# Kernel tuning notes

Measured on AMD Instinct MI355X. Metric: run time of the kernel, lower is better.

The kernel has to match this reference:

```python
import jax, jax.numpy as jnp
import numpy as np

N, F, H, C = 4096, 128, 32, 205   # nodes, in-features, hidden=32, clusters=ceil(4096/20)
L, T, R = 512, 12, 4              # teams, team size, replaced members per team
EPS_POOL = 1e-15                  # torch_geometric EPS in dense_diff_pool
BN_EPS = 1e-5


def setup_inputs():
    ks = jax.random.split(jax.random.key(0), 12)
    rng = np.random.default_rng(0)
    # distinct node ids per team; replace = first R members, remain = rest
    teams = np.argsort(rng.random((L, N)), axis=1)[:, :T].astype(np.int64)
    g = lambda i, shape, s: jax.random.normal(ks[i], shape, jnp.float32) * s
    D = 2 * H + C  # 269
    return {
        'x': g(0, (N, F), 1.0),
        'adj': jax.random.uniform(ks[1], (1, N, N), jnp.float32),
        'sample_teams': jnp.asarray(teams),
        'sample_replaces': jnp.asarray(teams[:, :R]),
        'W1r': g(2, (F, H), 0.08), 'b1': jnp.zeros((H,), jnp.float32), 'W1root': g(3, (F, H), 0.08),
        'g1': jnp.ones((H,), jnp.float32), 'be1': jnp.zeros((H,), jnp.float32),
        'W2r': g(4, (H, H), 0.17), 'b2': jnp.zeros((H,), jnp.float32), 'W2root': g(5, (H, H), 0.17),
        'g2': jnp.ones((H,), jnp.float32), 'be2': jnp.zeros((H,), jnp.float32),
        'W3r': g(6, (H, C), 0.17), 'b3': jnp.zeros((C,), jnp.float32), 'W3root': g(7, (H, C), 0.17),
        'g3': jnp.ones((C,), jnp.float32), 'be3': jnp.zeros((C,), jnp.float32),
        'Wl1': g(8, (D, C), 0.07), 'bl1': jnp.zeros((C,), jnp.float32),
    }


def _conv(x, adj, Wr, br, Wroot):
    # DenseGraphConv: lin_rel(adj @ x) + lin_root(x)  (lin_root has no bias)
    return jnp.matmul(adj, x) @ Wr + br + x @ Wroot


def _bn(x, gamma, beta):
    # BatchNorm1d in training mode over flattened (B*N, C)
    B, n, c = x.shape
    xf = x.reshape(-1, c)
    m = xf.mean(0)
    v = jnp.mean((xf - m) ** 2, axis=0)  # biased variance, as torch uses for normalization
    return (((xf - m) / jnp.sqrt(v + BN_EPS)) * gamma + beta).reshape(B, n, c)


def _rownorm(a, eps=1e-8):
    n = jnp.linalg.norm(a, axis=1, keepdims=True)
    return a / jnp.maximum(n, eps)


def reference(x, adj, sample_teams, sample_replaces, W1r, b1, W1root, g1, be1,
              W2r, b2, W2root, g2, be2, W3r, b3, W3root, g3, be3, Wl1, bl1):
    # GNN tower (relu before bn, matching self.bn(i, conv(...).relu()))
    x1 = _bn(jax.nn.relu(_conv(x, adj, W1r, b1, W1root)), g1, be1)    # [1,N,H]
    x2 = _bn(jax.nn.relu(_conv(x1, adj, W2r, b2, W2root)), g2, be2)   # [1,N,H]
    x3 = _bn(jax.nn.relu(_conv(x2, adj, W3r, b3, W3root)), g3, be3)   # [1,N,C]
    xcat = jnp.concatenate([x1, x2, x3], axis=-1)                     # [1,N,2H+C]
    s1 = jax.nn.softmax(jax.nn.relu(xcat @ Wl1 + bl1), axis=2)        # [1,N,C]

    # link-prediction style norm: || s1[0] @ s1[0]^T - adj ||_F
    tmp = s1[0] @ s1[0].T - adj                                       # [1,N,N]
    norm = jnp.sqrt(jnp.sum(tmp * tmp))

    # dense_diff_pool entropy loss (it re-softmaxes its input s)
    s2 = jax.nn.softmax(s1, axis=-1)
    e1 = jnp.mean(jnp.sum(-s2 * jnp.log(s2 + EPS_POOL), axis=-1))

    # similarity alignment: only the diagonal of sim_matrix(sim_x_mat, sim_s_mat) is summed
    xn = _rownorm(x)
    sn = _rownorm(s1[0])
    sim_x_mat = xn @ xn.T                                             # [N,N]
    sim_s_mat = sn @ sn.T                                             # [N,N]
    a_n = _rownorm(sim_x_mat)
    b_n = _rownorm(sim_s_mat)
    sim = -jnp.sum(a_n * b_n) / sim_x_mat.shape[0]

    # per-team replace/remain mean-embedding L1 loss (padded segment means)
    emb = xcat[0]                                                     # [N, 2H+C]
    rep = emb[sample_replaces].mean(axis=1)                           # [L, D]
    rem = emb[sample_teams[:, R:]].mean(axis=1)                       # [L, D]
    embedding_loss = jnp.mean(jnp.sum(jnp.abs(rep - rem), axis=-1))

    total_loss = 100.0 * norm + 10.0 * e1 + 100.0 * sim + embedding_loss
    return (s1, norm, e1, sim, total_loss, embedding_loss, emb)
```

## Files before the change

kernel.cpp:

```cpp
#include <hip/hip_runtime.h>
#include <math.h>

#define NN 4096
#define FF 128
#define HH 32
#define CC 205
#define DD 269
#define LL 512
#define TT 12
#define RR 4
#define KS 16
#define GP 208
#define DP 288
#define BST 40
#define GTS 224
#define SC(i) ((i) * 32)

typedef __attribute__((ext_vector_type(8))) short bf16x8;
typedef __attribute__((ext_vector_type(4))) float f32x4;
typedef __attribute__((ext_vector_type(8))) unsigned short u16x8;

__device__ __forceinline__ float wave_sum(float v) {
#pragma unroll
  for (int o = 32; o > 0; o >>= 1) v += __shfl_xor(v, o, 64);
  return v;
}
__device__ __forceinline__ float wave_max(float v) {
#pragma unroll
  for (int o = 32; o > 0; o >>= 1) v = fmaxf(v, __shfl_xor(v, o, 64));
  return v;
}
__device__ __forceinline__ unsigned short f2bf(float x) {
  union { float f; unsigned u; } v; v.f = x;
  unsigned r = v.u + 0x7FFFu + ((v.u >> 16) & 1u);
  return (unsigned short)(r >> 16);
}

__global__ __launch_bounds__(256) void k_prep(const float* __restrict__ x,
                                              const float* __restrict__ W1r,
                                              const float* __restrict__ W1root,
                                              const float* __restrict__ Wl1,
                                              unsigned short* __restrict__ mB,
                                              float* __restrict__ rootb,
                                              float* __restrict__ xn,
                                              unsigned short* __restrict__ xnR,
                                              unsigned short* __restrict__ xnB,
                                              unsigned short* __restrict__ Wl1T) {
  __shared__ float sX[32][132];
  __shared__ unsigned short sT[32][34];
  __shared__ unsigned short sT2[FF][34];
  const int tid = threadIdx.x;
  {
    const int i = blockIdx.x * 256 + tid;
    if (i < GP * DP) {
      const int c = i / DP, k = i - c * DP;
      Wl1T[i] = (c < CC && k < DD) ? f2bf(Wl1[(size_t)k * CC + c]) : (unsigned short)0;
    }
  }
  if (blockIdx.x < 128) {
    const int kb = blockIdx.x;
    for (int p = tid; p < 1024; p += 256) {
      const int node = p >> 5, c4 = p & 31;
      const float4 v = *reinterpret_cast<const float4*>(&x[((size_t)(kb * 32 + node)) * FF + c4 * 4]);
      sX[node][c4 * 4 + 0] = v.x; sX[node][c4 * 4 + 1] = v.y;
      sX[node][c4 * 4 + 2] = v.z; sX[node][c4 * 4 + 3] = v.w;
    }
    __syncthreads();
    const int c = tid & 31, g = tid >> 5;
    float a1[4] = {0.f, 0.f, 0.f, 0.f}, a2[4] = {0.f, 0.f, 0.f, 0.f};
    for (int k = 0; k < FF; ++k) {
      const float w1 = W1r[k * HH + c];
      const float w2 = W1root[k * HH + c];
#pragma unroll
      for (int ni = 0; ni < 4; ++ni) {
        const float av = sX[g * 4 + ni][k];
        a1[ni] = fmaf(av, w1, a1[ni]);
        a2[ni] = fmaf(av, w2, a2[ni]);
      }
    }
#pragma unroll
    for (int ni = 0; ni < 4; ++ni) {
      rootb[((size_t)kb * 32 + g * 4 + ni) * HH + c] = a2[ni];
      sT[c][g * 4 + ni] = f2bf(a1[ni]);
    }
    __syncthreads();
    if (tid < 128) {
      const int row = tid >> 2, seg = tid & 3;
      u16x8 v;
#pragma unroll
      for (int j = 0; j < 8; ++j) v[j] = sT[row][seg * 8 + j];
      *reinterpret_cast<u16x8*>(&mB[((size_t)kb * 32 + row) * 32 + seg * 8]) = v;
    }
  } else {
    const int kb = blockIdx.x - 128;
    const int lane = tid & 63;
    const int w = tid >> 6;
#pragma unroll
    for (int i = 0; i < 8; ++i) {
      const int node = w * 8 + i;
      const int row = kb * 32 + node;
      const float v0 = x[(size_t)row * FF + lane];
      const float v1 = x[(size_t)row * FF + 64 + lane];
      const float ss = wave_sum(v0 * v0 + v1 * v1);
      const float n = fmaxf(sqrtf(ss), 1e-8f);
      const float a = v0 / n, b = v1 / n;
      xn[(size_t)row * FF + lane] = a;
      xn[(size_t)row * FF + 64 + lane] = b;
      xnR[(size_t)row * FF + lane] = f2bf(a);
      xnR[(size_t)row * FF + 64 + lane] = f2bf(b);
      sT2[lane][node] = f2bf(a);
      sT2[64 + lane][node] = f2bf(b);
    }
    __syncthreads();
    const int rowc = tid >> 1, seg = (tid & 1) * 16;
    if (rowc < FF) {
      u16x8 a, b;
#pragma unroll
      for (int j = 0; j < 8; ++j) { a[j] = sT2[rowc][seg + j]; b[j] = sT2[rowc][seg + 8 + j]; }
      *reinterpret_cast<u16x8*>(&xnB[((size_t)kb * GP + rowc) * 32 + seg]) = a;
      *reinterpret_cast<u16x8*>(&xnB[((size_t)kb * GP + rowc) * 32 + seg + 8]) = b;
    }
  }
}

__global__ __launch_bounds__(256) void k_conv1f(const float* __restrict__ adj,
                                                unsigned short* __restrict__ adj_t,
                                                const unsigned short* __restrict__ mB,
                                                float* __restrict__ part,
                                                float* __restrict__ scalars) {
  __shared__ unsigned short sA[64][264];
  __shared__ float red[4];
  const int tid = threadIdx.x;
  const int rbase_blk = blockIdx.x * 64;
  const int kbase = blockIdx.y * 256;
  const int rb0 = blockIdx.x * 4;
  const int kb0 = blockIdx.y * 8;
  const int lane = tid & 63;
  const int w = tid >> 6;
  const int l15 = lane & 15;
  const int kgrp = (lane >> 4) * 8;
  bf16x8 bb0[8], bb1[8];
#pragma unroll
  for (int kt = 0; kt < 8; ++kt) {
    const size_t boff = ((size_t)(kb0 + kt) * 32) * 32;
    bb0[kt] = *reinterpret_cast<const bf16x8*>(&mB[boff + (size_t)l15 * 32 + kgrp]);
    bb1[kt] = *reinterpret_cast<const bf16x8*>(&mB[boff + (size_t)(16 + l15) * 32 + kgrp]);
  }
  float adjsq = 0.f;
#pragma unroll
  for (int i = 0; i < 16; ++i) {
    const int fi = i * 256 + tid;
    const int r = fi >> 6;
    const int c4 = fi & 63;
    const size_t goff = (size_t)(rbase_blk + r) * NN + kbase + c4 * 4;
    const float4 v = *reinterpret_cast<const float4*>(&adj[goff]);
    adjsq += v.x * v.x + v.y * v.y + v.z * v.z + v.w * v.w;
    ushort4 h;
    h.x = f2bf(v.x); h.y = f2bf(v.y); h.z = f2bf(v.z); h.w = f2bf(v.w);
    const size_t toff = ((size_t)(rb0 + (r >> 4)) * (NN / 32) + kb0 + (c4 >> 3)) * 512 +
                        (r & 15) * 32 + (c4 & 7) * 4;
    *reinterpret_cast<ushort4*>(&adj_t[toff]) = h;
    *reinterpret_cast<ushort4*>(&sA[r][c4 * 4]) = h;
  }
  __syncthreads();
  const int rloc = w * 16 + l15;
  f32x4 acc0 = {0.f, 0.f, 0.f, 0.f}, acc1 = {0.f, 0.f, 0.f, 0.f};
#pragma unroll
  for (int k0 = 0; k0 < 256; k0 += 32) {
    const bf16x8 a = *reinterpret_cast<const bf16x8*>(&sA[rloc][k0 + kgrp]);
    acc0 = __builtin_amdgcn_mfma_f32_16x16x32_bf16(a, bb0[k0 >> 5], acc0, 0, 0, 0);
    acc1 = __builtin_amdgcn_mfma_f32_16x16x32_bf16(a, bb1[k0 >> 5], acc1, 0, 0, 0);
  }
  float* pp = part + (size_t)blockIdx.y * (NN * HH);
  const int rout = rbase_blk + w * 16 + (lane >> 4) * 4;
#pragma unroll
  for (int r = 0; r < 4; ++r) {
    pp[(size_t)(rout + r) * HH + l15] = acc0[r];
    pp[(size_t)(rout + r) * HH + 16 + l15] = acc1[r];
  }
  adjsq = wave_sum(adjsq);
  if (lane == 0) red[w] = adjsq;
  __syncthreads();
  if (tid == 0) atomicAdd(&scalars[SC(1)], red[0] + red[1] + red[2] + red[3]);
}

__global__ __launch_bounds__(256) void k_adjmm(const unsigned short* __restrict__ adj_t,
                                               const unsigned short* __restrict__ mB,
                                               float* __restrict__ part) {
  const int tid = threadIdx.x;
  const int lane = tid & 63;
  const int w = tid >> 6;
  const int rb = blockIdx.x * 4 + w;
  const int kb0 = blockIdx.y * 8;
  const int l15 = lane & 15;
  const int kgrp = (lane >> 4) * 8;
  bf16x8 a[8], b0[8], b1[8];
#pragma unroll
  for (int kt = 0; kt < 8; ++kt) {
    const size_t aoff = ((size_t)rb * (NN / 32) + kb0 + kt) * 512;
    const size_t boff = ((size_t)(kb0 + kt) * 32) * 32;
    a[kt] = *reinterpret_cast<const bf16x8*>(&adj_t[aoff + l15 * 32 + kgrp]);
    b0[kt] = *reinterpret_cast<const bf16x8*>(&mB[boff + (size_t)l15 * 32 + kgrp]);
    b1[kt] = *reinterpret_cast<const bf16x8*>(&mB[boff + (size_t)(16 + l15) * 32 + kgrp]);
  }
  f32x4 acc0 = {0.f, 0.f, 0.f, 0.f}, acc1 = {0.f, 0.f, 0.f, 0.f};
#pragma unroll
  for (int kt = 0; kt < 8; ++kt) {
    acc0 = __builtin_amdgcn_mfma_f32_16x16x32_bf16(a[kt], b0[kt], acc0, 0, 0, 0);
    acc1 = __builtin_amdgcn_mfma_f32_16x16x32_bf16(a[kt], b1[kt], acc1, 0, 0, 0);
  }
  float* pp = part + (size_t)blockIdx.y * (NN * HH);
  const int rout = rb * 16 + (lane >> 4) * 4;
#pragma unroll
  for (int r = 0; r < 4; ++r) {
    pp[(size_t)(rout + r) * HH + l15] = acc0[r];
    pp[(size_t)(rout + r) * HH + 16 + l15] = acc1[r];
  }
}

__global__ __launch_bounds__(256) void k_epi32(const float* __restrict__ part,
                                               const float* __restrict__ bias,
                                               const float* __restrict__ root,
                                               float* __restrict__ t,
                                               float* __restrict__ colsum,
                                               float* __restrict__ colsq) {
  __shared__ float ls[HH], lq[HH];
  const int tid = threadIdx.x;
  const int idx = blockIdx.x * 256 + tid;
  const int c = idx & (HH - 1);
  if (tid < HH) { ls[tid] = 0.f; lq[tid] = 0.f; }
  __syncthreads();
  float s = bias[c] + root[idx];
#pragma unroll
  for (int sp = 0; sp < KS; ++sp) s += part[(size_t)sp * (NN * HH) + idx];
  s = fmaxf(s, 0.f);
  t[idx] = s;
  atomicAdd(&ls[c], s);
  atomicAdd(&lq[c], s * s);
  __syncthreads();
  if (tid < HH) {
    atomicAdd(&colsum[tid * 16], ls[tid]);
    atomicAdd(&colsq[tid * 16], lq[tid]);
  }
}

__global__ __launch_bounds__(256) void k_bnproj(const float* __restrict__ t,
                                                const float* __restrict__ colsum,
                                                const float* __restrict__ colsq,
                                                const float* __restrict__ g,
                                                const float* __restrict__ be,
                                                const float* __restrict__ W2r,
                                                const float* __restrict__ W2root,
                                                unsigned short* __restrict__ mB,
                                                float* __restrict__ rootb,
                                                float* __restrict__ emb) {
  __shared__ float sXf[32][33];
  __shared__ unsigned short sT[32][34];
  const int tid = threadIdx.x;
  const int kb = blockIdx.x;
  const int c = tid & 31, gq = tid >> 5;
  const float m = colsum[c * 16] * (1.f / NN);
  const float var = fmaxf(colsq[c * 16] * (1.f / NN) - m * m, 0.f);
  const float Ac = g[c] / sqrtf(var + 1e-5f);
  const float Bc = be[c] - m * Ac;
#pragma unroll
  for (int ni = 0; ni < 4; ++ni) {
    const int n = kb * 32 + gq * 4 + ni;
    const float v = fmaf(Ac, t[(size_t)n * HH + c], Bc);
    emb[(size_t)n * DD + c] = v;
    sXf[gq * 4 + ni][c] = v;
  }
  __syncthreads();
  float a1[4] = {0.f, 0.f, 0.f, 0.f}, a2[4] = {0.f, 0.f, 0.f, 0.f};
  for (int k = 0; k < HH; ++k) {
    const float w1 = W2r[k * HH + c];
    const float w2 = W2root[k * HH + c];
#pragma unroll
    for (int ni = 0; ni < 4; ++ni) {
      const float av = sXf[gq * 4 + ni][k];
      a1[ni] = fmaf(av, w1, a1[ni]);
      a2[ni] = fmaf(av, w2, a2[ni]);
    }
  }
#pragma unroll
  for (int ni = 0; ni < 4; ++ni) {
    rootb[((size_t)kb * 32 + gq * 4 + ni) * HH + c] = a2[ni];
    sT[c][gq * 4 + ni] = f2bf(a1[ni]);
  }
  __syncthreads();
  if (tid < 128) {
    const int row = tid >> 2, seg = tid & 3;
    u16x8 v;
#pragma unroll
    for (int j = 0; j < 8; ++j) v[j] = sT[row][seg * 8 + j];
    *reinterpret_cast<u16x8*>(&mB[((size_t)kb * 32 + row) * 32 + seg * 8]) = v;
  }
}

__global__ __launch_bounds__(256) void k_bnapply32(const float* __restrict__ t,
                                                   const float* __restrict__ colsum,
                                                   const float* __restrict__ colsq,
                                                   const float* __restrict__ g,
                                                   const float* __restrict__ be,
                                                   float* __restrict__ xo,
                                                   float* __restrict__ emb, int embOff,
                                                   unsigned short* __restrict__ xB) {
  __shared__ unsigned short sT[32][34];
  const int tid = threadIdx.x;
  const int kb = blockIdx.x;
  const int c = tid & 31, gq = tid >> 5;
  const float m = colsum[c * 16] * (1.f / NN);
  const float var = fmaxf(colsq[c * 16] * (1.f / NN) - m * m, 0.f);
  const float Ac = g[c] / sqrtf(var + 1e-5f);
  const float Bc = be[c] - m * Ac;
#pragma unroll
  for (int ni = 0; ni < 4; ++ni) {
    const int n = kb * 32 + gq * 4 + ni;
    const float v = fmaf(Ac, t[(size_t)n * HH + c], Bc);
    xo[(size_t)n * HH + c] = v;
    emb[(size_t)n * DD + embOff + c] = v;
    sT[c][gq * 4 + ni] = f2bf(v);
  }
  __syncthreads();
  if (tid < 128) {
    const int row = tid >> 2, seg = tid & 3;
    u16x8 o;
#pragma unroll
    for (int j = 0; j < 8; ++j) o[j] = sT[row][seg * 8 + j];
    *reinterpret_cast<u16x8*>(&xB[((size_t)kb * 32 + row) * 32 + seg * 8]) = o;
  }
}

__global__ __launch_bounds__(256) void k_epi3(const float* __restrict__ part,
                                              const float* __restrict__ W3r,
                                              const float* __restrict__ b3,
                                              const float* __restrict__ x2,
                                              const float* __restrict__ W3root,
                                              float* __restrict__ t3,
                                              float* __restrict__ colsum,
                                              float* __restrict__ colsq) {
  __shared__ float z[16][33];
  __shared__ float xr[16][33];
  const int row0 = blockIdx.x * 16;
  for (int s = threadIdx.x; s < 16 * 32; s += 256) {
    const int r = s >> 5, k = s & 31;
    float a = 0.f;
#pragma unroll
    for (int sp = 0; sp < KS; ++sp)
      a += part[(size_t)sp * (NN * HH) + (size_t)(row0 + r) * HH + k];
    z[r][k] = a;
    xr[r][k] = x2[(size_t)(row0 + r) * HH + k];
  }
  __syncthreads();
  const int c = threadIdx.x;
  if (c >= CC) return;
  float acc[16];
  const float bb = b3[c];
#pragma unroll
  for (int r = 0; r < 16; ++r) acc[r] = bb;
  for (int k = 0; k < 32; ++k) {
    const float w1 = W3r[k * CC + c];
    const float w2 = W3root[k * CC + c];
#pragma unroll
    for (int r = 0; r < 16; ++r) acc[r] += z[r][k] * w1 + xr[r][k] * w2;
  }
  float lsm = 0.f, lqm = 0.f;
#pragma unroll
  for (int r = 0; r < 16; ++r) {
    const float v = fmaxf(acc[r], 0.f);
    t3[(size_t)(row0 + r) * CC + c] = v;
    lsm += v;
    lqm += v * v;
  }
  atomicAdd(&colsum[c * 16], lsm);
  atomicAdd(&colsq[c * 16], lqm);
}

__global__ __launch_bounds__(256) void k_head(float* __restrict__ emb,
                                              const float* __restrict__ t3,
                                              const float* __restrict__ colsum3,
                                              const float* __restrict__ colsq3,
                                              const float* __restrict__ g3,
                                              const float* __restrict__ be3,
                                              const unsigned short* __restrict__ Wl1T,
                                              const float* __restrict__ bl1,
                                              float* __restrict__ s1,
                                              float* __restrict__ sn,
                                              unsigned short* __restrict__ s1B,
                                              unsigned short* __restrict__ snB,
                                              unsigned short* __restrict__ snR,
                                              float* __restrict__ scalars) {
  __shared__ unsigned short sA[16][296];
  __shared__ float lg[16][212];
  __shared__ unsigned short sTa[16][212];
  __shared__ unsigned short sTb[16][212];
  __shared__ float redE[4];
  const int tid = threadIdx.x;
  const int row0 = blockIdx.x * 16;
  for (int p = tid; p < 16 * 36; p += 256) {
    const int r = p / 36, ch = p - r * 36;
    const int row = row0 + r;
#pragma unroll
    for (int j = 0; j < 8; ++j) {
      const int d = ch * 8 + j;
      float v;
      if (d < 2 * HH) {
        v = emb[(size_t)row * DD + d];
      } else if (d < DD) {
        const int c3 = d - 2 * HH;
        const float m = colsum3[c3 * 16] * (1.f / NN);
        const float var = fmaxf(colsq3[c3 * 16] * (1.f / NN) - m * m, 0.f);
        const float Ac = g3[c3] / sqrtf(var + 1e-5f);
        const float Bc = be3[c3] - m * Ac;
        v = fmaf(Ac, t3[(size_t)row * CC + c3], Bc);
        emb[(size_t)row * DD + d] = v;
      } else {
        v = 0.f;
      }
      sA[r][d] = f2bf(v);
    }
  }
  __syncthreads();
  const int lane = tid & 63;
  const int w = tid >> 6;
  const int l15 = lane & 15;
  const int kgrp = (lane >> 4) * 8;
  {
    f32x4 acc[4];
#pragma unroll
    for (int i = 0; i < 4; ++i) acc[i] = (f32x4){0.f, 0.f, 0.f, 0.f};
#pragma unroll
    for (int i = 0; i < 4; ++i) {
      const int ct = w + i * 4;
      if (ct < 13) {
        const size_t brow = (size_t)(ct * 16 + l15) * DP;
#pragma unroll
        for (int k0 = 0; k0 < DP; k0 += 32) {
          const bf16x8 a = *reinterpret_cast<const bf16x8*>(&sA[l15][k0 + kgrp]);
          const bf16x8 b = *reinterpret_cast<const bf16x8*>(&Wl1T[brow + k0 + kgrp]);
          acc[i] = __builtin_amdgcn_mfma_f32_16x16x32_bf16(a, b, acc[i], 0, 0, 0);
        }
      }
    }
    const int lrow = (lane >> 4) * 4;
#pragma unroll
    for (int i = 0; i < 4; ++i) {
      const int ct = w + i * 4;
      if (ct < 13) {
#pragma unroll
        for (int r = 0; r < 4; ++r) lg[lrow + r][ct * 16 + l15] = acc[i][r];
      }
    }
  }
  __syncthreads();
  const int r0 = w * 4;
  const int c0 = lane * 4;
  const bool active = (c0 < GP);
  float bl[4];
#pragma unroll
  for (int j = 0; j < 4; ++j) bl[j] = (c0 + j < CC) ? bl1[c0 + j] : 0.f;
  float ent_acc = 0.f;
#pragma unroll
  for (int r = 0; r < 4; ++r) {
    const int lr = r0 + r;
    const int row = row0 + lr;
    float lgv[4] = {0.f, 0.f, 0.f, 0.f};
    if (active) {
#pragma unroll
      for (int j = 0; j < 4; ++j) lgv[j] = lg[lr][c0 + j];
    }
    float v[4];
    float ml = -1e30f;
#pragma unroll
    for (int j = 0; j < 4; ++j) {
      const int c = c0 + j;
      v[j] = (c < CC) ? fmaxf(lgv[j] + bl[j], 0.f) : -1e30f;
      ml = fmaxf(ml, v[j]);
    }
    const float m = wave_max(ml);
    float e[4];
    float sl = 0.f;
#pragma unroll
    for (int j = 0; j < 4; ++j) {
      const int c = c0 + j;
      e[j] = (c < CC) ? __expf(v[j] - m) : 0.f;
      sl += e[j];
    }
    const float S = wave_sum(sl);
    const float invS = 1.f / S;
    float p[4];
    float ql = 0.f;
#pragma unroll
    for (int j = 0; j < 4; ++j) {
      p[j] = e[j] * invS;
      ql += p[j] * p[j];
    }
    const float q = wave_sum(ql);
    const float inv = 1.f / fmaxf(sqrtf(q), 1e-8f);
    float m2l = -1e30f;
#pragma unroll
    for (int j = 0; j < 4; ++j) {
      const int c = c0 + j;
      if (c < CC) {
        s1[(size_t)row * CC + c] = p[j];
        sn[(size_t)row * CC + c] = p[j] * inv;
        m2l = fmaxf(m2l, p[j]);
      }
    }
    if (active) {
#pragma unroll
      for (int j = 0; j < 4; ++j) {
        const int c = c0 + j;
        const bool ok = (c < CC);
        sTa[lr][c] = ok ? f2bf(p[j]) : (unsigned short)0;
        sTb[lr][c] = ok ? f2bf(p[j] * inv) : (unsigned short)0;
      }
    }
    if (c0 < GTS) {
      ushort4 o;
      o.x = (c0 + 0 < CC) ? f2bf(p[0] * inv) : (unsigned short)0;
      o.y = (c0 + 1 < CC) ? f2bf(p[1] * inv) : (unsigned short)0;
      o.z = (c0 + 2 < CC) ? f2bf(p[2] * inv) : (unsigned short)0;
      o.w = (c0 + 3 < CC) ? f2bf(p[3] * inv) : (unsigned short)0;
      *reinterpret_cast<ushort4*>(&snR[(size_t)row * GTS + c0]) = o;
    }
    const float m2 = wave_max(m2l);
    float e2[4];
    float s2l = 0.f;
#pragma unroll
    for (int j = 0; j < 4; ++j) {
      const int c = c0 + j;
      e2[j] = (c < CC) ? __expf(p[j] - m2) : 0.f;
      s2l += e2[j];
    }
    const float S2 = wave_sum(s2l);
    const float invS2 = 1.f / S2;
    float tl = 0.f;
#pragma unroll
    for (int j = 0; j < 4; ++j) {
      const int c = c0 + j;
      if (c < CC) {
        const float sp = e2[j] * invS2;
        tl -= sp * logf(sp + 1e-15f);
      }
    }
    ent_acc += tl;
  }
  ent_acc = wave_sum(ent_acc);
  if (lane == 0) redE[w] = ent_acc;
  __syncthreads();
  if (tid == 0) atomicAdd(&scalars[SC(2)], redE[0] + redE[1] + redE[2] + redE[3]);
  if (tid < GP) {
    const int kb = row0 >> 5, no = row0 & 31;
    u16x8 oa0, ob0, oa1, ob1;
#pragma unroll
    for (int r = 0; r < 8; ++r) {
      oa0[r] = sTa[r][tid]; ob0[r] = sTb[r][tid];
      oa1[r] = sTa[8 + r][tid]; ob1[r] = sTb[8 + r][tid];
    }
    *reinterpret_cast<u16x8*>(&s1B[((size_t)kb * GP + tid) * 32 + no]) = oa0;
    *reinterpret_cast<u16x8*>(&s1B[((size_t)kb * GP + tid) * 32 + no + 8]) = oa1;
    *reinterpret_cast<u16x8*>(&snB[((size_t)kb * GP + tid) * 32 + no]) = ob0;
    *reinterpret_cast<u16x8*>(&snB[((size_t)kb * GP + tid) * 32 + no + 8]) = ob1;
  }
}

__global__ __launch_bounds__(512) void k_tail(const unsigned short* __restrict__ adj_t,
                                              const unsigned short* __restrict__ s1B,
                                              const float* __restrict__ s1,
                                              const unsigned short* __restrict__ xnB,
                                              const unsigned short* __restrict__ snB,
                                              unsigned short* __restrict__ GT0,
                                              unsigned short* __restrict__ GxsT,
                                              unsigned short* __restrict__ GsT,
                                              float* __restrict__ scalars) {
  const int tid = threadIdx.x;
  const int lane = tid & 63;
  const int w = tid >> 6;
  const int l15 = lane & 15;
  const int kgrp = (lane >> 4) * 8;
  if (blockIdx.x < 512) {
    __shared__ unsigned short sB[2][13][16][BST];
    __shared__ float red[8];
    const int bx = blockIdx.x & 31;
    const int ky = blockIdx.x >> 5;
    const int rb = bx * 8 + w;
    const int kb0 = ky * 8;
    const int g = lane >> 4;
    const int p0 = tid;
    const int ct0 = p0 >> 6, rr0 = (p0 >> 2) & 15, sg0 = (p0 & 3) * 8;
    const int p1 = tid + 512;
    const bool v1 = (p1 < 832);
    const int ct1 = p1 >> 6, rr1 = (p1 >> 2) & 15, sg1 = (p1 & 3) * 8;
    f32x4 acc[13];
#pragma unroll
    for (int ct = 0; ct < 13; ++ct) acc[ct] = (f32x4){0.f, 0.f, 0.f, 0.f};
    u16x8 st0, st1;
    st0 = *reinterpret_cast<const u16x8*>(&s1B[((size_t)kb0 * GP + ct0 * 16 + rr0) * 32 + sg0]);
    if (v1) st1 = *reinterpret_cast<const u16x8*>(&s1B[((size_t)kb0 * GP + ct1 * 16 + rr1) * 32 + sg1]);
    *reinterpret_cast<u16x8*>(&sB[0][ct0][rr0][sg0]) = st0;
    if (v1) *reinterpret_cast<u16x8*>(&sB[0][ct1][rr1][sg1]) = st1;
    __syncthreads();
    bf16x8 a = *reinterpret_cast<const bf16x8*>(
        &adj_t[((size_t)rb * (NN / 32) + kb0) * 512 + l15 * 32 + kgrp]);
    for (int kt = 0; kt < 8; ++kt) {
      const int cur = kt & 1;
      if (kt < 7) {
        const size_t kb = kb0 + kt + 1;
        st0 = *reinterpret_cast<const u16x8*>(&s1B[(kb * GP + ct0 * 16 + rr0) * 32 + sg0]);
        if (v1) st1 = *reinterpret_cast<const u16x8*>(&s1B[(kb * GP + ct1 * 16 + rr1) * 32 + sg1]);
      }
      bf16x8 a_next = a;
      if (kt < 7)
        a_next = *reinterpret_cast<const bf16x8*>(
            &adj_t[((size_t)rb * (NN / 32) + kb0 + kt + 1) * 512 + l15 * 32 + kgrp]);
#pragma unroll
      for (int ct = 0; ct < 13; ++ct) {
        const bf16x8 b = *reinterpret_cast<const bf16x8*>(&sB[cur][ct][l15][kgrp]);
        acc[ct] = __builtin_amdgcn_mfma_f32_16x16x32_bf16(a, b, acc[ct], 0, 0, 0);
      }
      if (kt < 7) {
        *reinterpret_cast<u16x8*>(&sB[cur ^ 1][ct0][rr0][sg0]) = st0;
        if (v1) *reinterpret_cast<u16x8*>(&sB[cur ^ 1][ct1][rr1][sg1]) = st1;
      }
      __syncthreads();
      a = a_next;
    }
    const int rout = rb * 16 + g * 4;
    float sc = 0.f;
#pragma unroll
    for (int ct = 0; ct < 13; ++ct) {
      const int col = ct * 16 + l15;
      if (col < CC) {
#pragma unroll
        for (int r = 0; r < 4; ++r)
          sc = fmaf(acc[ct][r], s1[(size_t)(rout + r) * CC + col], sc);
      }
    }
    sc = wave_sum(sc);
    if (lane == 0) red[w] = sc;
    __syncthreads();
    if (tid == 0) {
      float s = 0.f;
#pragma unroll
      for (int i = 0; i < 8; ++i) s += red[i];
      atomicAdd(&scalars[SC(0)], s);
    }
  } else {
    __shared__ float redg[8][16][17];
    __shared__ float redq[8];
    const int gb = blockIdx.x - 512;
    const int gid = gb / 169;
    const int rem = gb - gid * 169;
    const int tp = (rem % 13) * 16;
    const int tq = (rem / 13) * 16;
    const unsigned short *PT, *QT;
    unsigned short* GTout = nullptr;
    if (gid == 0)      { PT = xnB; QT = xnB; GTout = GT0;  if (tp >= FF || tq >= FF) return; }
    else if (gid == 1) { PT = xnB; QT = snB; GTout = GxsT; if (tp >= FF) return; }
    else if (gid == 2) { PT = snB; QT = snB; GTout = GsT; }
    else               { PT = s1B; QT = s1B; }
    f32x4 acc = {0.f, 0.f, 0.f, 0.f};
#pragma unroll 4
    for (int kt = 0; kt < 16; ++kt) {
      const int kb = w * 16 + kt;
      const bf16x8 a = *reinterpret_cast<const bf16x8*>(&PT[((size_t)kb * GP + tp + l15) * 32 + kgrp]);
      const bf16x8 b = *reinterpret_cast<const bf16x8*>(&QT[((size_t)kb * GP + tq + l15) * 32 + kgrp]);
      acc = __builtin_amdgcn_mfma_f32_16x16x32_bf16(a, b, acc, 0, 0, 0);
    }
    const int crow = (lane >> 4) * 4;
#pragma unroll
    for (int r = 0; r < 4; ++r) redg[w][crow + r][l15] = acc[r];
    __syncthreads();
    const int rr = tid >> 4, cc = tid & 15;
    if (gid == 3) {
      float q = 0.f;
      if (tid < 256) {
        float v = 0.f;
#pragma unroll
        for (int i = 0; i < 8; ++i) v += redg[i][rr][cc];
        q = v * v;
      }
      q = wave_sum(q);
      if (lane == 0) redq[w] = q;
      __syncthreads();
      if (tid == 0) {
        float s = 0.f;
#pragma unroll
        for (int i = 0; i < 8; ++i) s += redq[i];
        atomicAdd(&scalars[SC(5)], s);
      }
    } else {
      if (tid < 256) {
        float vt = 0.f;
#pragma unroll
        for (int i = 0; i < 8; ++i) vt += redg[i][cc][rr];
        GTout[(size_t)(tq + rr) * GTS + (tp + cc)] = f2bf(vt);
      }
    }
  }
}

__global__ __launch_bounds__(256) void k_rowsim(const unsigned short* __restrict__ xnR,
                                                const unsigned short* __restrict__ snR,
                                                const unsigned short* __restrict__ GT0,
                                                const unsigned short* __restrict__ GxsT,
                                                const unsigned short* __restrict__ GsT,
                                                const float* __restrict__ xn,
                                                const float* __restrict__ sn,
                                                float* __restrict__ scalars) {
  __shared__ unsigned short sX[16][136];
  __shared__ unsigned short sS[16][232];
  __shared__ float sH1[16][132];
  __shared__ float sU[16][212];
  __shared__ float sH2[16][212];
  __shared__ float redb[4];
  const int tid = threadIdx.x;
  const int row0 = blockIdx.x * 16;
  for (int p = tid; p < 16 * 16; p += 256) {
    const int r = p >> 4, ch = p & 15;
    *reinterpret_cast<u16x8*>(&sX[r][ch * 8]) =
        *reinterpret_cast<const u16x8*>(&xnR[(size_t)(row0 + r) * FF + ch * 8]);
  }
  for (int p = tid; p < 16 * 28; p += 256) {
    const int r = p / 28, ch = p - r * 28;
    *reinterpret_cast<u16x8*>(&sS[r][ch * 8]) =
        *reinterpret_cast<const u16x8*>(&snR[(size_t)(row0 + r) * GTS + ch * 8]);
  }
  __syncthreads();
  const int lane = tid & 63;
  const int w = tid >> 6;
  const int l15 = lane & 15;
  const int kgrp = (lane >> 4) * 8;
  const int lrow = (lane >> 4) * 4;
#pragma unroll
  for (int i = 0; i < 2; ++i) {
    const int ct = w + i * 4;
    f32x4 acc = {0.f, 0.f, 0.f, 0.f};
    const size_t brow = (size_t)(ct * 16 + l15) * GTS;
#pragma unroll
    for (int k0 = 0; k0 < FF; k0 += 32) {
      const bf16x8 a = *reinterpret_cast<const bf16x8*>(&sX[l15][k0 + kgrp]);
      const bf16x8 b = *reinterpret_cast<const bf16x8*>(&GT0[brow + k0 + kgrp]);
      acc = __builtin_amdgcn_mfma_f32_16x16x32_bf16(a, b, acc, 0, 0, 0);
    }
#pragma unroll
    for (int r = 0; r < 4; ++r) sH1[lrow + r][ct * 16 + l15] = acc[r];
  }
#pragma unroll
  for (int i = 0; i < 4; ++i) {
    const int ct = w + i * 4;
    if (ct < 13) {
      f32x4 acc = {0.f, 0.f, 0.f, 0.f};
      const size_t brow = (size_t)(ct * 16 + l15) * GTS;
#pragma unroll
      for (int k0 = 0; k0 < FF; k0 += 32) {
        const bf16x8 a = *reinterpret_cast<const bf16x8*>(&sX[l15][k0 + kgrp]);
        const bf16x8 b = *reinterpret_cast<const bf16x8*>(&GxsT[brow + k0 + kgrp]);
        acc = __builtin_amdgcn_mfma_f32_16x16x32_bf16(a, b, acc, 0, 0, 0);
      }
#pragma unroll
      for (int r = 0; r < 4; ++r) sU[lrow + r][ct * 16 + l15] = acc[r];
    }
  }
#pragma unroll
  for (int i = 0; i < 4; ++i) {
    const int ct = w + i * 4;
    if (ct < 13) {
      f32x4 acc = {0.f, 0.f, 0.f, 0.f};
      const size_t brow = (size_t)(ct * 16 + l15) * GTS;
#pragma unroll
      for (int k0 = 0; k0 < GTS; k0 += 32) {
        const bf16x8 a = *reinterpret_cast<const bf16x8*>(&sS[l15][k0 + kgrp]);
        const bf16x8 b = *reinterpret_cast<const bf16x8*>(&GsT[brow + k0 + kgrp]);
        acc = __builtin_amdgcn_mfma_f32_16x16x32_bf16(a, b, acc, 0, 0, 0);
      }
#pragma unroll
      for (int r = 0; r < 4; ++r) sH2[lrow + r][ct * 16 + l15] = acc[r];
    }
  }
  __syncthreads();
  float acc_sim = 0.f;
#pragma unroll
  for (int r = 0; r < 4; ++r) {
    const int lr = w * 4 + r;
    const int row = row0 + lr;
    float suu = 0.f, suv = 0.f, svv = 0.f;
#pragma unroll
    for (int c0 = 0; c0 < FF; c0 += 64) {
      suu = fmaf(xn[(size_t)row * FF + c0 + lane], sH1[lr][c0 + lane], suu);
    }
    for (int cb = lane; cb < CC; cb += 64) {
      const float sv = sn[(size_t)row * CC + cb];
      suv = fmaf(sU[lr][cb], sv, suv);
      svv = fmaf(sH2[lr][cb], sv, svv);
    }
    suu = wave_sum(suu);
    suv = wave_sum(suv);
    svv = wave_sum(svv);
    if (lane == 0) acc_sim += suv / sqrtf(suu * svv);
  }
  if (lane == 0) redb[w] = acc_sim;
  __syncthreads();
  if (tid == 0) atomicAdd(&scalars[SC(3)], redb[0] + redb[1] + redb[2] + redb[3]);
}

__global__ __launch_bounds__(256) void k_teams(const float* __restrict__ emb,
                                               const int* __restrict__ teams,
                                               const int* __restrict__ reps,
                                               float* __restrict__ scalars,
                                               unsigned int* __restrict__ ticket,
                                               float* __restrict__ outsc) {
  __shared__ float red[4];
  const int tid = threadIdx.x;
  const int team = blockIdx.x;
  float part = 0.f;
  for (int d = tid; d < DD; d += 256) {
    float a = 0.f, b = 0.f;
#pragma unroll
    for (int m = 0; m < RR; ++m) a += emb[(size_t)reps[team * RR + m] * DD + d];
#pragma unroll
    for (int m = RR; m < TT; ++m) b += emb[(size_t)teams[team * TT + m] * DD + d];
    part += fabsf(a * (1.f / RR) - b * (1.f / (TT - RR)));
  }
  part = wave_sum(part);
  if ((tid & 63) == 0) red[tid >> 6] = part;
  __syncthreads();
  if (tid == 0) {
    atomicAdd(&scalars[SC(4)], red[0] + red[1] + red[2] + red[3]);
    __threadfence();
    const unsigned int old = atomicAdd(ticket, 1u);
    if (old == (unsigned int)(LL - 1)) {
      const float trSAS = atomicAdd(&scalars[SC(0)], 0.f);
      const float adjsq = atomicAdd(&scalars[SC(1)], 0.f);
      const float ent   = atomicAdd(&scalars[SC(2)], 0.f);
      const float simS  = atomicAdd(&scalars[SC(3)], 0.f);
      const float embS  = atomicAdd(&scalars[SC(4)], 0.f);
      const float sumP2 = atomicAdd(&scalars[SC(5)], 0.f);
      const float normsq = fmaxf(sumP2 - 2.f * trSAS + adjsq, 0.f);
      const float norm = sqrtf(normsq);
      const float e1 = ent * (1.f / NN);
      const float sim = -simS * (1.f / NN);
      const float embl = embS * (1.f / LL);
      outsc[0] = norm;
      outsc[1] = e1;
      outsc[2] = sim;
      outsc[3] = 100.f * norm + 10.f * e1 + 100.f * sim + embl;
      outsc[4] = embl;
    }
  }
}

extern "C" void kernel_launch(void* const* d_in, const int* in_sizes, int n_in,
                              void* d_out, int out_size, void* d_ws, size_t ws_size,
                              hipStream_t stream) {
  const float* x      = (const float*)d_in[0];
  const float* adj    = (const float*)d_in[1];
  const int*   teams  = (const int*)d_in[2];
  const int*   reps   = (const int*)d_in[3];
  const float* W1r    = (const float*)d_in[4];
  const float* b1     = (const float*)d_in[5];
  const float* W1root = (const float*)d_in[6];
  const float* g1     = (const float*)d_in[7];
  const float* be1    = (const float*)d_in[8];
  const float* W2r    = (const float*)d_in[9];
  const float* b2     = (const float*)d_in[10];
  const float* W2root = (const float*)d_in[11];
  const float* g2     = (const float*)d_in[12];
  const float* be2    = (const float*)d_in[13];
  const float* W3r    = (const float*)d_in[14];
  const float* b3     = (const float*)d_in[15];
  const float* W3root = (const float*)d_in[16];
  const float* g3     = (const float*)d_in[17];
  const float* be3    = (const float*)d_in[18];
  const float* Wl1    = (const float*)d_in[19];
  const float* bl1    = (const float*)d_in[20];

  char* wp = (char*)d_ws;
  auto alloc = [&](size_t bytes) { char* p = wp; wp += (bytes + 255) & ~(size_t)255; return p; };
  unsigned short* adj_t = (unsigned short*)alloc((size_t)NN * NN * 2);
  unsigned short* mB    = (unsigned short*)alloc((size_t)HH * NN * 2);
  unsigned short* x2B   = (unsigned short*)alloc((size_t)HH * NN * 2);
  unsigned short* s1B   = (unsigned short*)alloc((size_t)GP * NN * 2);
  unsigned short* snB   = (unsigned short*)alloc((size_t)GP * NN * 2);
  unsigned short* Wl1T  = (unsigned short*)alloc((size_t)GP * DP * 2);
  unsigned short* xnR   = (unsigned short*)alloc((size_t)NN * FF * 2);
  unsigned short* snR   = (unsigned short*)alloc((size_t)NN * GTS * 2);
  float* rootb  = (float*)alloc((size_t)NN * HH * 4);
  float* t      = (float*)alloc((size_t)NN * HH * 4);
  float* x2     = (float*)alloc((size_t)NN * HH * 4);
  float* part   = (float*)alloc((size_t)KS * NN * HH * 4);
  float* t3     = (float*)alloc((size_t)NN * CC * 4);
  float* sn     = (float*)alloc((size_t)NN * CC * 4);
  float* xn     = (float*)alloc((size_t)NN * FF * 4);
  float* scalars = (float*)alloc(256 * 4);
  float* colsum1 = (float*)alloc(512 * 4);
  float* colsq1  = (float*)alloc(512 * 4);
  float* colsum2 = (float*)alloc(512 * 4);
  float* colsq2  = (float*)alloc(512 * 4);
  float* colsum3 = (float*)alloc(4096 * 4);
  float* colsq3  = (float*)alloc(4096 * 4);
  unsigned short* GTall = (unsigned short*)alloc((size_t)3 * GP * GTS * 2);
  unsigned short* xnB   = (unsigned short*)alloc((size_t)GP * NN * 2);
  char* zero_end = wp;
  unsigned short* GT0   = GTall;
  unsigned short* GxsT  = GTall + (size_t)GP * GTS;
  unsigned short* GsT   = GTall + (size_t)2 * GP * GTS;
  unsigned int* ticket = (unsigned int*)&scalars[SC(6)];
  (void)ws_size; (void)in_sizes; (void)n_in; (void)out_size;

  float* out   = (float*)d_out;
  float* s1    = out;
  float* outsc = out + (size_t)NN * CC;
  float* emb   = out + (size_t)NN * CC + 5;

  hipMemsetAsync(scalars, 0, (size_t)(zero_end - (char*)scalars), stream);

  k_prep<<<256, 256, 0, stream>>>(x, W1r, W1root, Wl1, mB, rootb, xn, xnR, xnB, Wl1T);

  k_conv1f<<<dim3(NN / 64, KS), 256, 0, stream>>>(adj, adj_t, mB, part, scalars);
  k_epi32<<<NN * HH / 256, 256, 0, stream>>>(part, b1, rootb, t, colsum1, colsq1);
  k_bnproj<<<NN / 32, 256, 0, stream>>>(t, colsum1, colsq1, g1, be1, W2r, W2root, mB, rootb, emb);

  k_adjmm<<<dim3(NN / 64, KS), 256, 0, stream>>>(adj_t, mB, part);
  k_epi32<<<NN * HH / 256, 256, 0, stream>>>(part, b2, rootb, t, colsum2, colsq2);
  k_bnapply32<<<NN / 32, 256, 0, stream>>>(t, colsum2, colsq2, g2, be2, x2, emb, HH, x2B);

  k_adjmm<<<dim3(NN / 64, KS), 256, 0, stream>>>(adj_t, x2B, part);
  k_epi3<<<NN / 16, 256, 0, stream>>>(part, W3r, b3, x2, W3root, t3, colsum3, colsq3);

  k_head<<<NN / 16, 256, 0, stream>>>(emb, t3, colsum3, colsq3, g3, be3, Wl1T, bl1,
                                      s1, sn, s1B, snB, snR, scalars);

  k_tail<<<512 + 676, 512, 0, stream>>>(adj_t, s1B, s1, xnB, snB, GT0, GxsT, GsT, scalars);

  k_rowsim<<<NN / 16, 256, 0, stream>>>(xnR, snR, GT0, GxsT, GsT, xn, sn, scalars);
  k_teams<<<LL, 256, 0, stream>>>(emb, teams, reps, scalars, ticket, outsc);
}
```

Before: 213.2 us.

## Fuse split-K adj matmuls with epilogues via in-block LDS reduction

Replaces the 16-way split-K adjacency matmuls, which wrote fp32 partials to global memory, and their separate epilogue kernels with one kernel per conv layer. Each 512-thread block now owns 16 rows and the full K range: its 8 waves each cover a K slice and reduce through shared memory, then apply bias, root term, ReLU and the column statistics (or the layer-3 projection) in place. This removes the 8 MB partial buffer traffic and three kernel launches. The cost is a grid of only 256 blocks with little parallelism each, and conv1 now streams adj in sequential chunks with two barriers per chunk, which may reduce memory-level parallelism on the largest read.

```diff
diff --git a/kernel.cpp b/kernel.cpp
--- a/kernel.cpp
+++ b/kernel.cpp
@@ -9,7 +9,6 @@
 #define LL 512
 #define TT 12
 #define RR 4
-#define KS 16
 #define GP 208
 #define DP 288
 #define BST 40
@@ -123,125 +122,236 @@
   }
 }
 
-__global__ __launch_bounds__(256) void k_conv1f(const float* __restrict__ adj,
-                                                unsigned short* __restrict__ adj_t,
-                                                const unsigned short* __restrict__ mB,
-                                                float* __restrict__ part,
-                                                float* __restrict__ scalars) {
-  __shared__ unsigned short sA[64][264];
-  __shared__ float red[4];
+__global__ __launch_bounds__(512) void k_conv1(const float* __restrict__ adj,
+                                               unsigned short* __restrict__ adj_t,
+                                               const unsigned short* __restrict__ mB,
+                                               const float* __restrict__ bias,
+                                               const float* __restrict__ root,
+                                               float* __restrict__ t,
+                                               float* __restrict__ colsum,
+                                               float* __restrict__ colsq,
+                                               float* __restrict__ scalars) {
+  __shared__ unsigned short sA[16][520];
+  __shared__ float sRed[8][16][33];
+  __shared__ float ls[HH], lq[HH];
+  __shared__ float redsq[8];
   const int tid = threadIdx.x;
-  const int rbase_blk = blockIdx.x * 64;
-  const int kbase = blockIdx.y * 256;
-  const int rb0 = blockIdx.x * 4;
-  const int kb0 = blockIdx.y * 8;
   const int lane = tid & 63;
   const int w = tid >> 6;
   const int l15 = lane & 15;
   const int kgrp = (lane >> 4) * 8;
-  bf16x8 bb0[8], bb1[8];
-#pragma unroll
-  for (int kt = 0; kt < 8; ++kt) {
-    const size_t boff = ((size_t)(kb0 + kt) * 32) * 32;
-    bb0[kt] = *reinterpret_cast<const bf16x8*>(&mB[boff + (size_t)l15 * 32 + kgrp]);
-    bb1[kt] = *reinterpret_cast<const bf16x8*>(&mB[boff + (size_t)(16 + l15) * 32 + kgrp]);
-  }
+  const int rb = blockIdx.x;
+  const int row0 = rb * 16;
   float adjsq = 0.f;
-#pragma unroll
-  for (int i = 0; i < 16; ++i) {
-    const int fi = i * 256 + tid;
-    const int r = fi >> 6;
-    const int c4 = fi & 63;
-    const size_t goff = (size_t)(rbase_blk + r) * NN + kbase + c4 * 4;
-    const float4 v = *reinterpret_cast<const float4*>(&adj[goff]);
-    adjsq += v.x * v.x + v.y * v.y + v.z * v.z + v.w * v.w;
-    ushort4 h;
-    h.x = f2bf(v.x); h.y = f2bf(v.y); h.z = f2bf(v.z); h.w = f2bf(v.w);
-    const size_t toff = ((size_t)(rb0 + (r >> 4)) * (NN / 32) + kb0 + (c4 >> 3)) * 512 +
-                        (r & 15) * 32 + (c4 & 7) * 4;
-    *reinterpret_cast<ushort4*>(&adj_t[toff]) = h;
-    *reinterpret_cast<ushort4*>(&sA[r][c4 * 4]) = h;
-  }
-  __syncthreads();
-  const int rloc = w * 16 + l15;
   f32x4 acc0 = {0.f, 0.f, 0.f, 0.f}, acc1 = {0.f, 0.f, 0.f, 0.f};
-#pragma unroll
-  for (int k0 = 0; k0 < 256; k0 += 32) {
-    const bf16x8 a = *reinterpret_cast<const bf16x8*>(&sA[rloc][k0 + kgrp]);
-    acc0 = __builtin_amdgcn_mfma_f32_16x16x32_bf16(a, bb0[k0 >> 5], acc0, 0, 0, 0);
-    acc1 = __builtin_amdgcn_mfma_f32_16x16x32_bf16(a, bb1[k0 >> 5], acc1, 0, 0, 0);
-  }
-  float* pp = part + (size_t)blockIdx.y * (NN * HH);
-  const int rout = rbase_blk + w * 16 + (lane >> 4) * 4;
+  for (int chunk = 0; chunk < 8; ++chunk) {
+    const int kbase = chunk * 512;
+#pragma unroll
+    for (int i = 0; i < 4; ++i) {
+      const int fi = i * 512 + tid;
+      const int r = fi >> 7;
+      const int c4 = fi & 127;
+      const size_t goff = (size_t)(row0 + r) * NN + kbase + c4 * 4;
+      const float4 v = *reinterpret_cast<const float4*>(&adj[goff]);
+      adjsq += v.x * v.x + v.y * v.y + v.z * v.z + v.w * v.w;
+      ushort4 h;
+      h.x = f2bf(v.x); h.y = f2bf(v.y); h.z = f2bf(v.z); h.w = f2bf(v.w);
+      const size_t toff = ((size_t)rb * (NN / 32) + (kbase >> 5) + (c4 >> 3)) * 512 +
+                          r * 32 + (c4 & 7) * 4;
+      *reinterpret_cast<ushort4*>(&adj_t[toff]) = h;
+      *reinterpret_cast<ushort4*>(&sA[r][c4 * 4]) = h;
+    }
+    __syncthreads();
+#pragma unroll
+    for (int j = 0; j < 2; ++j) {
+      const int ktl = w * 2 + j;
+      const bf16x8 a = *reinterpret_cast<const bf16x8*>(&sA[l15][ktl * 32 + kgrp]);
+      const size_t boff = (size_t)(chunk * 16 + ktl) * 1024;
+      const bf16x8 b0 = *reinterpret_cast<const bf16x8*>(&mB[boff + l15 * 32 + kgrp]);
+      const bf16x8 b1v = *reinterpret_cast<const bf16x8*>(&mB[boff + (16 + l15) * 32 + kgrp]);
+      acc0 = __builtin_amdgcn_mfma_f32_16x16x32_bf16(a, b0, acc0, 0, 0, 0);
+      acc1 = __builtin_amdgcn_mfma_f32_16x16x32_bf16(a, b1v, acc1, 0, 0, 0);
+    }
+    __syncthreads();
+  }
+  const int crow = (lane >> 4) * 4;
 #pragma unroll
   for (int r = 0; r < 4; ++r) {
-    pp[(size_t)(rout + r) * HH + l15] = acc0[r];
-    pp[(size_t)(rout + r) * HH + 16 + l15] = acc1[r];
-  }
+    sRed[w][crow + r][l15] = acc0[r];
+    sRed[w][crow + r][16 + l15] = acc1[r];
+  }
+  if (tid < HH) { ls[tid] = 0.f; lq[tid] = 0.f; }
   adjsq = wave_sum(adjsq);
-  if (lane == 0) red[w] = adjsq;
-  __syncthreads();
-  if (tid == 0) atomicAdd(&scalars[SC(1)], red[0] + red[1] + red[2] + red[3]);
-}
-
-__global__ __launch_bounds__(256) void k_adjmm(const unsigned short* __restrict__ adj_t,
+  if (lane == 0) redsq[w] = adjsq;
+  __syncthreads();
+  {
+    const int r = tid >> 5, c = tid & 31;
+    float v = 0.f;
+#pragma unroll
+    for (int i = 0; i < 8; ++i) v += sRed[i][r][c];
+    const int n = row0 + r;
+    float s = bias[c] + root[(size_t)n * HH + c] + v;
+    s = fmaxf(s, 0.f);
+    t[(size_t)n * HH + c] = s;
+    atomicAdd(&ls[c], s);
+    atomicAdd(&lq[c], s * s);
+  }
+  __syncthreads();
+  if (tid < HH) {
+    atomicAdd(&colsum[tid * 16], ls[tid]);
+    atomicAdd(&colsq[tid * 16], lq[tid]);
+  }
+  if (tid == 0) {
+    float s = 0.f;
+#pragma unroll
+    for (int i = 0; i < 8; ++i) s += redsq[i];
+    atomicAdd(&scalars[SC(1)], s);
+  }
+}
+
+__global__ __launch_bounds__(512) void k_conv2(const unsigned short* __restrict__ adj_t,
                                                const unsigned short* __restrict__ mB,
-                                               float* __restrict__ part) {
-  const int tid = threadIdx.x;
-  const int lane = tid & 63;
-  const int w = tid >> 6;
-  const int rb = blockIdx.x * 4 + w;
-  const int kb0 = blockIdx.y * 8;
-  const int l15 = lane & 15;
-  const int kgrp = (lane >> 4) * 8;
-  bf16x8 a[8], b0[8], b1[8];
-#pragma unroll
-  for (int kt = 0; kt < 8; ++kt) {
-    const size_t aoff = ((size_t)rb * (NN / 32) + kb0 + kt) * 512;
-    const size_t boff = ((size_t)(kb0 + kt) * 32) * 32;
-    a[kt] = *reinterpret_cast<const bf16x8*>(&adj_t[aoff + l15 * 32 + kgrp]);
-    b0[kt] = *reinterpret_cast<const bf16x8*>(&mB[boff + (size_t)l15 * 32 + kgrp]);
-    b1[kt] = *reinterpret_cast<const bf16x8*>(&mB[boff + (size_t)(16 + l15) * 32 + kgrp]);
-  }
-  f32x4 acc0 = {0.f, 0.f, 0.f, 0.f}, acc1 = {0.f, 0.f, 0.f, 0.f};
-#pragma unroll
-  for (int kt = 0; kt < 8; ++kt) {
-    acc0 = __builtin_amdgcn_mfma_f32_16x16x32_bf16(a[kt], b0[kt], acc0, 0, 0, 0);
-    acc1 = __builtin_amdgcn_mfma_f32_16x16x32_bf16(a[kt], b1[kt], acc1, 0, 0, 0);
-  }
-  float* pp = part + (size_t)blockIdx.y * (NN * HH);
-  const int rout = rb * 16 + (lane >> 4) * 4;
-#pragma unroll
-  for (int r = 0; r < 4; ++r) {
-    pp[(size_t)(rout + r) * HH + l15] = acc0[r];
-    pp[(size_t)(rout + r) * HH + 16 + l15] = acc1[r];
-  }
-}
-
-__global__ __launch_bounds__(256) void k_epi32(const float* __restrict__ part,
                                                const float* __restrict__ bias,
                                                const float* __restrict__ root,
                                                float* __restrict__ t,
                                                float* __restrict__ colsum,
                                                float* __restrict__ colsq) {
+  __shared__ float sRed[8][16][33];
   __shared__ float ls[HH], lq[HH];
   const int tid = threadIdx.x;
-  const int idx = blockIdx.x * 256 + tid;
-  const int c = idx & (HH - 1);
+  const int lane = tid & 63;
+  const int w = tid >> 6;
+  const int l15 = lane & 15;
+  const int kgrp = (lane >> 4) * 8;
+  const int rb = blockIdx.x;
+  const int row0 = rb * 16;
+  const int kb0 = w * 16;
+  f32x4 acc0 = {0.f, 0.f, 0.f, 0.f}, acc1 = {0.f, 0.f, 0.f, 0.f};
+#pragma unroll
+  for (int h = 0; h < 2; ++h) {
+    bf16x8 a[8], b0[8], b1v[8];
+#pragma unroll
+    for (int kt = 0; kt < 8; ++kt) {
+      const int kb = kb0 + h * 8 + kt;
+      const size_t aoff = ((size_t)rb * (NN / 32) + kb) * 512;
+      const size_t boff = (size_t)kb * 1024;
+      a[kt] = *reinterpret_cast<const bf16x8*>(&adj_t[aoff + l15 * 32 + kgrp]);
+      b0[kt] = *reinterpret_cast<const bf16x8*>(&mB[boff + (size_t)l15 * 32 + kgrp]);
+      b1v[kt] = *reinterpret_cast<const bf16x8*>(&mB[boff + (size_t)(16 + l15) * 32 + kgrp]);
+    }
+#pragma unroll
+    for (int kt = 0; kt < 8; ++kt) {
+      acc0 = __builtin_amdgcn_mfma_f32_16x16x32_bf16(a[kt], b0[kt], acc0, 0, 0, 0);
+      acc1 = __builtin_amdgcn_mfma_f32_16x16x32_bf16(a[kt], b1v[kt], acc1, 0, 0, 0);
+    }
+  }
+  const int crow = (lane >> 4) * 4;
+#pragma unroll
+  for (int r = 0; r < 4; ++r) {
+    sRed[w][crow + r][l15] = acc0[r];
+    sRed[w][crow + r][16 + l15] = acc1[r];
+  }
   if (tid < HH) { ls[tid] = 0.f; lq[tid] = 0.f; }
   __syncthreads();
-  float s = bias[c] + root[idx];
-#pragma unroll
-  for (int sp = 0; sp < KS; ++sp) s += part[(size_t)sp * (NN * HH) + idx];
-  s = fmaxf(s, 0.f);
-  t[idx] = s;
-  atomicAdd(&ls[c], s);
-  atomicAdd(&lq[c], s * s);
+  {
+    const int r = tid >> 5, c = tid & 31;
+    float v = 0.f;
+#pragma unroll
+    for (int i = 0; i < 8; ++i) v += sRed[i][r][c];
+    const int n = row0 + r;
+    float s = bias[c] + root[(size_t)n * HH + c] + v;
+    s = fmaxf(s, 0.f);
+    t[(size_t)n * HH + c] = s;
+    atomicAdd(&ls[c], s);
+    atomicAdd(&lq[c], s * s);
+  }
   __syncthreads();
   if (tid < HH) {
     atomicAdd(&colsum[tid * 16], ls[tid]);
     atomicAdd(&colsq[tid * 16], lq[tid]);
   }
+}
+
+__global__ __launch_bounds__(512) void k_conv3(const unsigned short* __restrict__ adj_t,
+                                               const unsigned short* __restrict__ x2B,
+                                               const float* __restrict__ W3r,
+                                               const float* __restrict__ b3,
+                                               const float* __restrict__ x2,
+                                               const float* __restrict__ W3root,
+                                               float* __restrict__ t3,
+                                               float* __restrict__ colsum,
+                                               float* __restrict__ colsq) {
+  __shared__ float sRed[8][16][33];
+  __shared__ float sZ[16][33];
+  __shared__ float sXr[16][33];
+  const int tid = threadIdx.x;
+  const int lane = tid & 63;
+  const int w = tid >> 6;
+  const int l15 = lane & 15;
+  const int kgrp = (lane >> 4) * 8;
+  const int rb = blockIdx.x;
+  const int row0 = rb * 16;
+  const int kb0 = w * 16;
+  f32x4 acc0 = {0.f, 0.f, 0.f, 0.f}, acc1 = {0.f, 0.f, 0.f, 0.f};
+#pragma unroll
+  for (int h = 0; h < 2; ++h) {
+    bf16x8 a[8], b0[8], b1v[8];
+#pragma unroll
+    for (int kt = 0; kt < 8; ++kt) {
+      const int kb = kb0 + h * 8 + kt;
+      const size_t aoff = ((size_t)rb * (NN / 32) + kb) * 512;
+      const size_t boff = (size_t)kb * 1024;
+      a[kt] = *reinterpret_cast<const bf16x8*>(&adj_t[aoff + l15 * 32 + kgrp]);
+      b0[kt] = *reinterpret_cast<const bf16x8*>(&x2B[boff + (size_t)l15 * 32 + kgrp]);
+      b1v[kt] = *reinterpret_cast<const bf16x8*>(&x2B[boff + (size_t)(16 + l15) * 32 + kgrp]);
+    }
+#pragma unroll
+    for (int kt = 0; kt < 8; ++kt) {
+      acc0 = __builtin_amdgcn_mfma_f32_16x16x32_bf16(a[kt], b0[kt], acc0, 0, 0, 0);
+      acc1 = __builtin_amdgcn_mfma_f32_16x16x32_bf16(a[kt], b1v[kt], acc1, 0, 0, 0);
+    }
+  }
+  const int crow = (lane >> 4) * 4;
+#pragma unroll
+  for (int r = 0; r < 4; ++r) {
+    sRed[w][crow + r][l15] = acc0[r];
+    sRed[w][crow + r][16 + l15] = acc1[r];
+  }
+  {
+    const int r = tid >> 5, c = tid & 31;
+    sXr[r][c] = x2[(size_t)(row0 + r) * HH + c];
+  }
+  __syncthreads();
+  {
+    const int r = tid >> 5, c = tid & 31;
+    float v = 0.f;
+#pragma unroll
+    for (int i = 0; i < 8; ++i) v += sRed[i][r][c];
+    sZ[r][c] = v;
+  }
+  __syncthreads();
+  const int c = tid;
+  if (c >= CC) return;
+  float acc[16];
+  const float bb = b3[c];
+#pragma unroll
+  for (int r = 0; r < 16; ++r) acc[r] = bb;
+  for (int k = 0; k < 32; ++k) {
+    const float w1 = W3r[k * CC + c];
+    const float w2 = W3root[k * CC + c];
+#pragma unroll
+    for (int r = 0; r < 16; ++r) acc[r] += sZ[r][k] * w1 + sXr[r][k] * w2;
+  }
+  float lsm = 0.f, lqm = 0.f;
+#pragma unroll
+  for (int r = 0; r < 16; ++r) {
+    const float v = fmaxf(acc[r], 0.f);
+    t3[(size_t)(row0 + r) * CC + c] = v;
+    lsm += v;
+    lqm += v * v;
+  }
+  atomicAdd(&colsum[c * 16], lsm);
+  atomicAdd(&colsq[c * 16], lqm);
 }
 
 __global__ __launch_bounds__(256) void k_bnproj(const float* __restrict__ t,
@@ -329,51 +439,6 @@
     for (int j = 0; j < 8; ++j) o[j] = sT[row][seg * 8 + j];
     *reinterpret_cast<u16x8*>(&xB[((size_t)kb * 32 + row) * 32 + seg * 8]) = o;
   }
-}
-
-__global__ __launch_bounds__(256) void k_epi3(const float* __restrict__ part,
-                                              const float* __restrict__ W3r,
-                                              const float* __restrict__ b3,
-                                              const float* __restrict__ x2,
-                                              const float* __restrict__ W3root,
-                                              float* __restrict__ t3,
-                                              float* __restrict__ colsum,
-                                              float* __restrict__ colsq) {
-  __shared__ float z[16][33];
-  __shared__ float xr[16][33];
-  const int row0 = blockIdx.x * 16;
-  for (int s = threadIdx.x; s < 16 * 32; s += 256) {
-    const int r = s >> 5, k = s & 31;
-    float a = 0.f;
-#pragma unroll
-    for (int sp = 0; sp < KS; ++sp)
-      a += part[(size_t)sp * (NN * HH) + (size_t)(row0 + r) * HH + k];
-    z[r][k] = a;
-    xr[r][k] = x2[(size_t)(row0 + r) * HH + k];
-  }
-  __syncthreads();
-  const int c = threadIdx.x;
-  if (c >= CC) return;
-  float acc[16];
-  const float bb = b3[c];
-#pragma unroll
-  for (int r = 0; r < 16; ++r) acc[r] = bb;
-  for (int k = 0; k < 32; ++k) {
-    const float w1 = W3r[k * CC + c];
-    const float w2 = W3root[k * CC + c];
-#pragma unroll
-    for (int r = 0; r < 16; ++r) acc[r] += z[r][k] * w1 + xr[r][k] * w2;
-  }
-  float lsm = 0.f, lqm = 0.f;
-#pragma unroll
-  for (int r = 0; r < 16; ++r) {
-    const float v = fmaxf(acc[r], 0.f);
-    t3[(size_t)(row0 + r) * CC + c] = v;
-    lsm += v;
-    lqm += v * v;
-  }
-  atomicAdd(&colsum[c * 16], lsm);
-  atomicAdd(&colsq[c * 16], lqm);
 }
 
 __global__ __launch_bounds__(256) void k_head(float* __restrict__ emb,
@@ -889,7 +954,6 @@
   float* rootb  = (float*)alloc((size_t)NN * HH * 4);
   float* t      = (float*)alloc((size_t)NN * HH * 4);
   float* x2     = (float*)alloc((size_t)NN * HH * 4);
-  float* part   = (float*)alloc((size_t)KS * NN * HH * 4);
   float* t3     = (float*)alloc((size_t)NN * CC * 4);
   float* sn     = (float*)alloc((size_t)NN * CC * 4);
   float* xn     = (float*)alloc((size_t)NN * FF * 4);
@@ -918,16 +982,13 @@
 
   k_prep<<<256, 256, 0, stream>>>(x, W1r, W1root, Wl1, mB, rootb, xn, xnR, xnB, Wl1T);
 
-  k_conv1f<<<dim3(NN / 64, KS), 256, 0, stream>>>(adj, adj_t, mB, part, scalars);
-  k_epi32<<<NN * HH / 256, 256, 0, stream>>>(part, b1, rootb, t, colsum1, colsq1);
+  k_conv1<<<256, 512, 0, stream>>>(adj, adj_t, mB, b1, rootb, t, colsum1, colsq1, scalars);
   k_bnproj<<<NN / 32, 256, 0, stream>>>(t, colsum1, colsq1, g1, be1, W2r, W2root, mB, rootb, emb);
 
-  k_adjmm<<<dim3(NN / 64, KS), 256, 0, stream>>>(adj_t, mB, part);
-  k_epi32<<<NN * HH / 256, 256, 0, stream>>>(part, b2, rootb, t, colsum2, colsq2);
+  k_conv2<<<256, 512, 0, stream>>>(adj_t, mB, b2, rootb, t, colsum2, colsq2);
   k_bnapply32<<<NN / 32, 256, 0, stream>>>(t, colsum2, colsq2, g2, be2, x2, emb, HH, x2B);
 
-  k_adjmm<<<dim3(NN / 64, KS), 256, 0, stream>>>(adj_t, x2B, part);
-  k_epi3<<<NN / 16, 256, 0, stream>>>(part, W3r, b3, x2, W3root, t3, colsum3, colsq3);
+  k_conv3<<<256, 512, 0, stream>>>(adj_t, x2B, W3r, b3, x2, W3root, t3, colsum3, colsq3);
 
   k_head<<<NN / 16, 256, 0, stream>>>(emb, t3, colsum3, colsq3, g3, be3, Wl1T, bl1,
                                       s1, sn, s1B, snB, snR, scalars);
```

Result: faster. 189.8 us (-10.9%).
